# Optimization experiments

Hardware: AMD Instinct MI355X
Metric: run time of the kernel (lower is better)

The kernel has to match this reference:

```python
import jax, jax.numpy as jnp
import numpy as np

B, T, IN, H, S, OUT = 128, 512, 64, 1024, 64, 1


def _lstm_cell(x, h, c, Wih, Whh, bih, bhh):
    # PyTorch gate order: i, f, g, o
    z = x @ Wih.T + h @ Whh.T + bih + bhh  # (B, 4H)
    i, f, g, o = jnp.split(z, 4, axis=-1)
    c = jax.nn.sigmoid(f) * c + jax.nn.sigmoid(i) * jnp.tanh(g)
    h = jax.nn.sigmoid(o) * jnp.tanh(c)
    return h, c


def _run_layer(xs, Wih, Whh, bih, bhh):
    # xs: (T, B, in); returns (ys (T,B,H), h_final, c_final)
    b = xs.shape[1]
    h0 = jnp.zeros((b, H), xs.dtype)
    c0 = jnp.zeros((b, H), xs.dtype)

    def step(carry, x):
        h, c = carry
        h, c = _lstm_cell(x, h, c, Wih, Whh, bih, bhh)
        return (h, c), h

    (hf, cf), ys = jax.lax.scan(step, (h0, c0), xs)
    return ys, hf, cf


def setup_inputs() -> dict:
    key = jax.random.key(0)
    ks = jax.random.split(key, 20)
    s = 0.02
    d = {"x": jax.random.normal(ks[0], (B, T, IN), jnp.float32)}
    # encoder params
    d["enc_Wih0"] = jax.random.normal(ks[1], (4 * H, IN), jnp.float32) * s
    d["enc_Whh0"] = jax.random.normal(ks[2], (4 * H, H), jnp.float32) * s
    d["enc_bih0"] = jnp.zeros((4 * H,), jnp.float32)
    d["enc_bhh0"] = jnp.zeros((4 * H,), jnp.float32)
    d["enc_Wih1"] = jax.random.normal(ks[3], (4 * H, H), jnp.float32) * s
    d["enc_Whh1"] = jax.random.normal(ks[4], (4 * H, H), jnp.float32) * s
    d["enc_bih1"] = jnp.zeros((4 * H,), jnp.float32)
    d["enc_bhh1"] = jnp.zeros((4 * H,), jnp.float32)
    # decoder params (input size = OUT = 1)
    d["dec_Wih0"] = jax.random.normal(ks[5], (4 * H, OUT), jnp.float32) * s
    d["dec_Whh0"] = jax.random.normal(ks[6], (4 * H, H), jnp.float32) * s
    d["dec_bih0"] = jnp.zeros((4 * H,), jnp.float32)
    d["dec_bhh0"] = jnp.zeros((4 * H,), jnp.float32)
    d["dec_Wih1"] = jax.random.normal(ks[7], (4 * H, H), jnp.float32) * s
    d["dec_Whh1"] = jax.random.normal(ks[8], (4 * H, H), jnp.float32) * s
    d["dec_bih1"] = jnp.zeros((4 * H,), jnp.float32)
    d["dec_bhh1"] = jnp.zeros((4 * H,), jnp.float32)
    d["fc_W"] = jax.random.normal(ks[9], (OUT, H), jnp.float32) * s
    d["fc_b"] = jnp.zeros((OUT,), jnp.float32)
    return d


def reference(x, enc_Wih0, enc_Whh0, enc_bih0, enc_bhh0,
              enc_Wih1, enc_Whh1, enc_bih1, enc_bhh1,
              dec_Wih0, dec_Whh0, dec_bih0, dec_bhh0,
              dec_Wih1, dec_Whh1, dec_bih1, dec_bhh1,
              fc_W, fc_b):
    b = x.shape[0]
    xs = jnp.transpose(x, (1, 0, 2))  # (T, B, IN)
    # encoder: layer-by-layer
    ys0, h0e, c0e = _run_layer(xs, enc_Wih0, enc_Whh0, enc_bih0, enc_bhh0)
    _, h1e, c1e = _run_layer(ys0, enc_Wih1, enc_Whh1, enc_bih1, enc_bhh1)

    inp0 = jnp.zeros((b, OUT), x.dtype)

    def dec_step(carry, _):
        h0, c0, h1, c1, inp = carry
        h0, c0 = _lstm_cell(inp, h0, c0, dec_Wih0, dec_Whh0, dec_bih0, dec_bhh0)
        h1, c1 = _lstm_cell(h0, h1, c1, dec_Wih1, dec_Whh1, dec_bih1, dec_bhh1)
        out = h1 @ fc_W.T + fc_b  # (B, OUT)
        return (h0, c0, h1, c1, out), out

    _, outs = jax.lax.scan(dec_step, (h0e, c0e, h1e, c1e, inp0), None, length=S)
    return jnp.transpose(outs, (1, 0, 2))  # (B, S, OUT)
```

## Files before the change

### kernel.cpp

```cpp
#include <hip/hip_runtime.h>
#include <cmath>
#include <cstdint>
#include <cstddef>

#define BB   128
#define TT   512
#define INF  64
#define HH   1024
#define NG   4096
#define SS   64
#define NBLK 192
#define NTHR 512

#define SWHI_B 0
#define SLO_B  131072
#define LDS_BYTES 155648

#define LO_SCALE   2048.0f
#define LO_UNSCALE 4.8828125e-4f

typedef __attribute__((ext_vector_type(8))) short sh8;
typedef __attribute__((ext_vector_type(4))) float f32x4;

__device__ __forceinline__ float h2f(unsigned short u) {
  return (float)__builtin_bit_cast(_Float16, u);
}
__device__ __forceinline__ unsigned short f2h(float f) {
  return __builtin_bit_cast(unsigned short, (_Float16)f);
}
__device__ __forceinline__ float sigm(float x) { return 1.f / (1.f + __expf(-x)); }
__device__ __forceinline__ float tanh_f(float x) {
  x = fminf(15.f, fmaxf(-15.f, x));
  const float e = __expf(2.f * x);
  return (e - 1.f) / (e + 1.f);
}
__device__ __forceinline__ sh8 ld8(const unsigned short* p) { return *(const sh8*)p; }

__device__ __forceinline__ void ld8sc(sh8& d, const unsigned short* p) {
  asm volatile("global_load_dwordx4 %0, %1, off sc0 sc1" : "=v"(d) : "v"(p));
}
__device__ __forceinline__ void ldx4sc(f32x4& d, const float* p) {
  asm volatile("global_load_dwordx4 %0, %1, off sc0 sc1" : "=v"(d) : "v"(p));
}
__device__ __forceinline__ void stx4sc(float* p, f32x4 v) {
  asm volatile("global_store_dwordx4 %0, %1, off sc0 sc1" :: "v"(p), "v"(v) : "memory");
}
__device__ __forceinline__ void st16sc(unsigned short* p, unsigned int v) {
  asm volatile("global_store_short %0, %1, off sc0 sc1" :: "v"(p), "v"(v) : "memory");
}
__device__ __forceinline__ void waitvm(int n) {
  if (n == 6)       asm volatile("s_waitcnt vmcnt(6)" ::: "memory");
  else if (n == 3)  asm volatile("s_waitcnt vmcnt(3)" ::: "memory");
  else              asm volatile("s_waitcnt vmcnt(0)" ::: "memory");
  __builtin_amdgcn_sched_barrier(0);
}

__device__ __forceinline__ void block_sync_lds() {
  asm volatile("s_waitcnt lgkmcnt(0)" ::: "memory");
  __builtin_amdgcn_s_barrier();
  asm volatile("" ::: "memory");
}

#if defined(__HIP_DEVICE_COMPILE__)
typedef __attribute__((ext_vector_type(8))) _Float16 hf8;
template <class T> T&& my_declval();
template <class V, class = void> struct mfma_takes { static constexpr bool value = false; };
template <class V>
struct mfma_takes<V, decltype((void)__builtin_amdgcn_mfma_f32_16x16x32_f16(
                        my_declval<V>(), my_declval<V>(), my_declval<f32x4>(), 0, 0, 0))> {
  static constexpr bool value = true;
};
template <class V>
__device__ __forceinline__ f32x4 mfma_imp(V a, V b, f32x4 c) {
  return __builtin_amdgcn_mfma_f32_16x16x32_f16(a, b, c, 0, 0, 0);
}
__device__ __forceinline__ f32x4 mfma_f16(sh8 a, sh8 b, f32x4 c) {
  if constexpr (mfma_takes<sh8>::value) {
    return mfma_imp<sh8>(a, b, c);
  } else {
    return mfma_imp<hf8>(__builtin_bit_cast(hf8, a), __builtin_bit_cast(hf8, b), c);
  }
}
#else
__device__ __forceinline__ f32x4 mfma_f16(sh8, sh8, f32x4 c) { return c; }
#endif

__global__ __launch_bounds__(256) void prep_weight(const float* __restrict__ W,
                                                   unsigned short* __restrict__ hi,
                                                   unsigned short* __restrict__ lo,
                                                   int lk) {
  const int K = 1 << lk;
  const int idx = blockIdx.x * 256 + threadIdx.x;
  if (idx >= (NG << lk)) return;
  const int n = idx >> lk;
  const int k = idx & (K - 1);
  const float v = W[idx];
  const unsigned short h = f2h(v);
  const unsigned short l = f2h((v - h2f(h)) * LO_SCALE);
  const int nkch = K >> 5;
  const size_t o =
      ((((size_t)(n >> 4) * nkch + (k >> 5)) * 64) + (((k >> 3) & 3) * 16) + (n & 15)) * 8 +
      (k & 7);
  hi[o] = h;
  lo[o] = l;
}

__global__ __launch_bounds__(256) void prep_bias(const float* __restrict__ a,
                                                 const float* __restrict__ b,
                                                 float* __restrict__ o) {
  const int i = blockIdx.x * 256 + threadIdx.x;
  if (i < NG) o[i] = a[i] + b[i];
}

__global__ __launch_bounds__(256) void init_out(float* __restrict__ out_tmp,
                                                const float* __restrict__ fcb) {
  const int i = blockIdx.x * 256 + threadIdx.x;
  if (i < SS * BB) out_tmp[i] = fcb[0];
}

struct KArgs {
  const float* x;
  const unsigned short *wih0_h, *wih0_l;
  const unsigned short *whh0e_h, *whh0e_l;
  const unsigned short *wih1e_h, *wih1e_l;
  const unsigned short *whh1e_h, *whh1e_l;
  const unsigned short *whh0d_h, *whh0d_l;
  const unsigned short *wih1d_h, *wih1d_l;
  const unsigned short *whh1d_h, *whh1d_l;
  const float *bias0e, *bias1e, *bias0d, *bias1d;
  const float *w0col, *fcw, *fcb;
  unsigned short *h00, *h01;
  unsigned short *h10, *h11;
  float *zb0, *zb1;
  float *out_tmp;
  float *outp;
  int *arrive;
};

__device__ __forceinline__ void gbar(int* arrive, int it) {
  asm volatile("s_waitcnt vmcnt(0)" ::: "memory");
  __syncthreads();
  const int tid = threadIdx.x;
  if (tid == 0)
    __hip_atomic_store(&arrive[blockIdx.x * 16], it, __ATOMIC_RELAXED, __HIP_MEMORY_SCOPE_AGENT);
  if (tid < NBLK) {
    while (__hip_atomic_load(&arrive[tid * 16], __ATOMIC_RELAXED, __HIP_MEMORY_SCOPE_AGENT) < it)
      __builtin_amdgcn_s_sleep(1);
  }
  __syncthreads();
  asm volatile("" ::: "memory");
}

__device__ __forceinline__ void load_whi(unsigned short* lds, const unsigned short* hi, int jt) {
#pragma unroll
  for (int g = 0; g < 4; ++g) {
    const uint4* src = (const uint4*)(hi + ((size_t)(g * 64 + jt) * 32) * 512);
    uint4* dst = (uint4*)((char*)lds + SWHI_B + g * 32768);
    for (int u = threadIdx.x; u < 2048; u += NTHR) dst[u] = src[u];
  }
}

__device__ __forceinline__ const unsigned short* lo_src(const unsigned short* glo, int jt,
                                                        int c, int f) {
  const int g = f >> 7, rem = f & 127, kcl = rem >> 6, l = rem & 63;
  const size_t u16 = ((size_t)((g * 64 + jt) * 32) + c * 2 + kcl) * 64 + l;
  return glo + u16 * 8;
}

__device__ __forceinline__ void issue_chunk(const unsigned short* arh,
                                            const unsigned short* glo, int jt, int c, int kg,
                                            int tid, int wid, unsigned short* lds,
                                            sh8 (&AH)[2]) {
#pragma unroll
  for (int kcl = 0; kcl < 2; ++kcl)
    ld8sc(AH[kcl], arh + c * 64 + kcl * 32 + kg * 8);
  __builtin_amdgcn_global_load_lds(
      (const void*)lo_src(glo, jt, c, tid),
      (void*)((char*)lds + SLO_B + (c % 3) * 8192 + wid * 1024), 16, 0, 0);
}

__device__ __forceinline__ void compute_chunk(f32x4* acc, f32x4* accL,
                                              const unsigned short* lds, int c, int lane,
                                              const sh8 (&AH)[2]) {
#pragma unroll
  for (int kcl = 0; kcl < 2; ++kcl) {
    const int kc = c * 2 + kcl;
#pragma unroll
    for (int g = 0; g < 4; ++g) {
      const sh8 bH = ld8(lds + (g * 32 + kc) * 512 + lane * 8);
      const sh8 bL = ld8(lds + SLO_B / 2 + (c % 3) * 4096 + (g * 2 + kcl) * 512 + lane * 8);
      acc[g] = mfma_f16(AH[kcl], bH, acc[g]);
      accL[g] = mfma_f16(AH[kcl], bL, accL[g]);
    }
  }
}

__device__ __forceinline__ void gemm1024(f32x4* acc, f32x4* accL,
                                         const unsigned short* __restrict__ ah,
                                         const unsigned short* __restrict__ glo,
                                         int jt, unsigned short* lds) {
  const int tid = threadIdx.x;
  const int lane = tid & 63, wid = tid >> 6;
  const int kg = lane >> 4;
  const int arow = wid * 16 + (lane & 15);
  const unsigned short* arh = ah + (size_t)arow * HH;

  sh8 AH[3][2];

  asm volatile("s_waitcnt vmcnt(0)" ::: "memory");
  issue_chunk(arh, glo, jt, 0, kg, tid, wid, lds, AH[0]);
  issue_chunk(arh, glo, jt, 1, kg, tid, wid, lds, AH[1]);
  issue_chunk(arh, glo, jt, 2, kg, tid, wid, lds, AH[2]);
  waitvm(6);
  block_sync_lds();

#pragma unroll
  for (int c = 0; c < 16; ++c) {
    compute_chunk(acc, accL, lds, c, lane, AH[c % 3]);
    if (c < 15) {
      waitvm(c <= 13 ? 3 : 0);
      block_sync_lds();
      if (c + 3 < 16)
        issue_chunk(arh, glo, jt, c + 3, kg, tid, wid, lds, AH[c % 3]);
    }
  }
}

__device__ __forceinline__ void combine(f32x4* acc, const f32x4* accL) {
#pragma unroll
  for (int g = 0; g < 4; ++g) acc[g] += accL[g] * LO_UNSCALE;
}

__device__ __forceinline__ void gemm_x(f32x4* acc, f32x4* accL, const float* __restrict__ x,
                                       int t, const unsigned short* __restrict__ wxh,
                                       const unsigned short* __restrict__ wxl, int jt) {
  const int tid = threadIdx.x;
  const int lane = tid & 63, wid = tid >> 6;
  const int kg = lane >> 4;
  const int arow = wid * 16 + (lane & 15);
  const float* xr = x + (size_t)arow * (TT * INF) + t * INF;
#pragma unroll
  for (int kc2 = 0; kc2 < 2; ++kc2) {
    const int kb = kc2 * 32 + kg * 8;
    sh8 xh, xl;
#pragma unroll
    for (int e = 0; e < 8; ++e) {
      const float v = xr[kb + e];
      const unsigned short h = f2h(v);
      xh[e] = (short)h;
      xl[e] = (short)f2h((v - h2f(h)) * LO_SCALE);
    }
#pragma unroll
    for (int g = 0; g < 4; ++g) {
      const size_t bo = (((size_t)(g * 64 + jt) * 2 + kc2) * 64 + lane) * 8;
      const sh8 bH = ld8(wxh + bo);
      const sh8 bL = ld8(wxl + bo);
      acc[g] = mfma_f16(xh, bH, acc[g]);
      accL[g] = mfma_f16(xl, bH, accL[g]);
      accL[g] = mfma_f16(xh, bL, accL[g]);
    }
  }
}

__device__ __forceinline__ void store_z(f32x4* acc, float* zb, int jt) {
  const int tid = threadIdx.x;
  const int lane = tid & 63, wid = tid >> 6;
  const int col = lane & 15, kg = lane >> 4;
#pragma unroll
  for (int g = 0; g < 4; ++g) {
    const int row = g * HH + jt * 16 + col;
    const int bq = wid * 16 + kg * 4;
    stx4sc(zb + (size_t)row * BB + bq, acc[g]);
  }
}
__device__ __forceinline__ void add_z(f32x4* acc, const float* zb, int jt) {
  const int tid = threadIdx.x;
  const int lane = tid & 63, wid = tid >> 6;
  const int col = lane & 15, kg = lane >> 4;
  f32x4 t0, t1, t2, t3;
  const int bq = wid * 16 + kg * 4;
  ldx4sc(t0, zb + (size_t)(0 * HH + jt * 16 + col) * BB + bq);
  ldx4sc(t1, zb + (size_t)(1 * HH + jt * 16 + col) * BB + bq);
  ldx4sc(t2, zb + (size_t)(2 * HH + jt * 16 + col) * BB + bq);
  ldx4sc(t3, zb + (size_t)(3 * HH + jt * 16 + col) * BB + bq);
  asm volatile("s_waitcnt vmcnt(0)" ::: "memory");
  __builtin_amdgcn_sched_barrier(0);
  acc[0] += t0;
  acc[1] += t1;
  acc[2] += t2;
  acc[3] += t3;
}

template <int MODE>
__device__ __forceinline__ void cellfin(f32x4* acc, float* creg,
                                        const float* __restrict__ bias, int jt,
                                        unsigned short* __restrict__ nh,
                                        const float* w0g, const float* inp_vec, float fcwj,
                                        float* fc_out) {
  const int tid = threadIdx.x;
  const int lane = tid & 63, wid = tid >> 6;
  const int col = lane & 15, kg = lane >> 4;
  const int j = jt * 16 + col;
  const float b0 = bias[j], b1 = bias[HH + j], b2 = bias[2 * HH + j], b3 = bias[3 * HH + j];
#pragma unroll
  for (int r = 0; r < 4; ++r) {
    const int b = wid * 16 + kg * 4 + r;
    float zi = acc[0][r] + b0;
    float zf = acc[1][r] + b1;
    float zg = acc[2][r] + b2;
    float zo = acc[3][r] + b3;
    if constexpr (MODE == 1) {
      const float ip = inp_vec
          ? __hip_atomic_load(inp_vec + b, __ATOMIC_RELAXED, __HIP_MEMORY_SCOPE_AGENT)
          : 0.f;
      zi += ip * w0g[0];
      zf += ip * w0g[1];
      zg += ip * w0g[2];
      zo += ip * w0g[3];
    }
    const float cn = sigm(zf) * creg[r] + sigm(zi) * tanh_f(zg);
    const float hn = sigm(zo) * tanh_f(cn);
    creg[r] = cn;
    st16sc(nh + (size_t)b * HH + j, f2h(hn));
    if constexpr (MODE == 2) {
      float cb = hn * fcwj;
      cb += __shfl_xor(cb, 1);
      cb += __shfl_xor(cb, 2);
      cb += __shfl_xor(cb, 4);
      cb += __shfl_xor(cb, 8);
      if (col == 0) atomicAdd(fc_out + b, cb);
    }
  }
}

__device__ __forceinline__ void zacc(f32x4* acc) {
#pragma unroll
  for (int g = 0; g < 4; ++g) acc[g] = f32x4{0.f, 0.f, 0.f, 0.f};
}

__global__ __launch_bounds__(NTHR, 2) void seq2seq_coop(KArgs a) {
  extern __shared__ unsigned short lds[];
  const int bid = blockIdx.x;
  const int role = bid >> 6;
  const int jt = bid & 63;
  const int tid = threadIdx.x;
  int bseq = 0;

  unsigned short* h0[2] = {a.h00, a.h01};
  unsigned short* h1[2] = {a.h10, a.h11};
  float* zb[2] = {a.zb0, a.zb1};

  if (role == 0) load_whi(lds, a.whh0e_h, jt);
  else if (role == 1) load_whi(lds, a.wih1e_h, jt);
  else load_whi(lds, a.whh1e_h, jt);
  __syncthreads();

  float creg[4] = {};

  for (int i = 0; i < TT + 2; ++i) {
    if (role == 0) {
      if (i < TT) {
        f32x4 acc[4], accL[4];
        zacc(acc);
        zacc(accL);
        gemm1024(acc, accL, h0[(i + 1) & 1], a.whh0e_l, jt, lds);
        gemm_x(acc, accL, a.x, i, a.wih0_h, a.wih0_l, jt);
        combine(acc, accL);
        cellfin<0>(acc, creg, a.bias0e, jt, h0[i & 1], nullptr, nullptr, 0.f, nullptr);
      }
    } else if (role == 1) {
      if (i >= 1 && i <= TT) {
        const int s = i - 1;
        f32x4 acc[4], accL[4];
        zacc(acc);
        zacc(accL);
        gemm1024(acc, accL, h0[s & 1], a.wih1e_l, jt, lds);
        combine(acc, accL);
        store_z(acc, zb[s & 1], jt);
      }
    } else {
      if (i >= 2) {
        const int s = i - 2;
        f32x4 acc[4], accL[4];
        zacc(acc);
        zacc(accL);
        gemm1024(acc, accL, h1[(s + 1) & 1], a.whh1e_l, jt, lds);
        combine(acc, accL);
        add_z(acc, zb[s & 1], jt);
        cellfin<0>(acc, creg, a.bias1e, jt, h1[s & 1], nullptr, nullptr, 0.f, nullptr);
      }
    }
    gbar(a.arrive, ++bseq);
  }

  if (role == 0) load_whi(lds, a.whh0d_h, jt);
  else if (role == 1) load_whi(lds, a.wih1d_h, jt);
  else load_whi(lds, a.whh1d_h, jt);
  __syncthreads();

  float w0g[4] = {0.f, 0.f, 0.f, 0.f};
  float fcwj = 0.f;
  if (role == 0) {
    const int j = jt * 16 + (tid & 15);
    w0g[0] = a.w0col[j];
    w0g[1] = a.w0col[HH + j];
    w0g[2] = a.w0col[2 * HH + j];
    w0g[3] = a.w0col[3 * HH + j];
  }
  if (role == 2) fcwj = a.fcw[jt * 16 + (tid & 15)];

  for (int s = 0; s < SS; ++s) {
    f32x4 acc2[4], accL2[4];
    if (role == 2) {
      zacc(acc2);
      zacc(accL2);
      gemm1024(acc2, accL2, h1[(s + 1) & 1], a.whh1d_l, jt, lds);
      combine(acc2, accL2);
    }
    if (role == 0) {
      f32x4 acc[4], accL[4];
      zacc(acc);
      zacc(accL);
      gemm1024(acc, accL, h0[(s + 1) & 1], a.whh0d_l, jt, lds);
      combine(acc, accL);
      cellfin<1>(acc, creg, a.bias0d, jt, h0[s & 1], w0g,
                 s ? a.out_tmp + (s - 1) * BB : nullptr, 0.f, nullptr);
    }
    gbar(a.arrive, ++bseq);
    if (role == 1) {
      f32x4 acc[4], accL[4];
      zacc(acc);
      zacc(accL);
      gemm1024(acc, accL, h0[s & 1], a.wih1d_l, jt, lds);
      combine(acc, accL);
      store_z(acc, zb[0], jt);
    }
    gbar(a.arrive, ++bseq);
    if (role == 2) {
      add_z(acc2, zb[0], jt);
      cellfin<2>(acc2, creg, a.bias1d, jt, h1[s & 1], nullptr, nullptr, fcwj,
                 a.out_tmp + s * BB);
    }
    gbar(a.arrive, ++bseq);
  }

  if (bid < 16) {
    const int gi = bid * NTHR + tid;
    const int b = gi >> 6, s2 = gi & 63;
    a.outp[gi] =
        __hip_atomic_load(a.out_tmp + s2 * BB + b, __ATOMIC_RELAXED, __HIP_MEMORY_SCOPE_AGENT);
  }
}

extern "C" void kernel_launch(void* const* d_in, const int* in_sizes, int n_in,
                              void* d_out, int out_size, void* d_ws, size_t ws_size,
                              hipStream_t stream) {
  (void)in_sizes; (void)n_in; (void)out_size; (void)ws_size;
  const float* x     = (const float*)d_in[0];
  const float* eWih0 = (const float*)d_in[1];
  const float* eWhh0 = (const float*)d_in[2];
  const float* eBih0 = (const float*)d_in[3];
  const float* eBhh0 = (const float*)d_in[4];
  const float* eWih1 = (const float*)d_in[5];
  const float* eWhh1 = (const float*)d_in[6];
  const float* eBih1 = (const float*)d_in[7];
  const float* eBhh1 = (const float*)d_in[8];
  const float* dWih0 = (const float*)d_in[9];
  const float* dWhh0 = (const float*)d_in[10];
  const float* dBih0 = (const float*)d_in[11];
  const float* dBhh0 = (const float*)d_in[12];
  const float* dWih1 = (const float*)d_in[13];
  const float* dWhh1 = (const float*)d_in[14];
  const float* dBih1 = (const float*)d_in[15];
  const float* dBhh1 = (const float*)d_in[16];
  const float* fcW   = (const float*)d_in[17];
  const float* fcB   = (const float*)d_in[18];
  float* out = (float*)d_out;

  char* base = (char*)d_ws;
  size_t off = 0;
  auto alloc = [&](size_t bytes) -> void* {
    void* p = base + off;
    off = (off + bytes + 255) & ~(size_t)255;
    return p;
  };

  unsigned short* h00 = (unsigned short*)alloc(BB * HH * 2);
  unsigned short* h01 = (unsigned short*)alloc(BB * HH * 2);
  unsigned short* h10 = (unsigned short*)alloc(BB * HH * 2);
  unsigned short* h11 = (unsigned short*)alloc(BB * HH * 2);
  int* bar = (int*)alloc(NBLK * 16 * sizeof(int));
  const size_t zbytes = off;

  float* zb0 = (float*)alloc((size_t)NG * BB * 4);
  float* zb1 = (float*)alloc((size_t)NG * BB * 4);
  float* out_tmp = (float*)alloc(SS * BB * 4);

  unsigned short* wih0_h = (unsigned short*)alloc((size_t)NG * INF * 2);
  unsigned short* wih0_l = (unsigned short*)alloc((size_t)NG * INF * 2);
  auto big = [&]() { return (unsigned short*)alloc((size_t)NG * HH * 2); };
  unsigned short *whh0e_h = big(), *whh0e_l = big();
  unsigned short *wih1e_h = big(), *wih1e_l = big();
  unsigned short *whh1e_h = big(), *whh1e_l = big();
  unsigned short *whh0d_h = big(), *whh0d_l = big();
  unsigned short *wih1d_h = big(), *wih1d_l = big();
  unsigned short *whh1d_h = big(), *whh1d_l = big();
  float* bias0e = (float*)alloc(NG * 4);
  float* bias1e = (float*)alloc(NG * 4);
  float* bias0d = (float*)alloc(NG * 4);
  float* bias1d = (float*)alloc(NG * 4);

  (void)hipMemsetAsync(base, 0, zbytes, stream);
  const int gb = (NG * HH + 255) / 256;
  prep_weight<<<gb, 256, 0, stream>>>(eWhh0, whh0e_h, whh0e_l, 10);
  prep_weight<<<gb, 256, 0, stream>>>(eWih1, wih1e_h, wih1e_l, 10);
  prep_weight<<<gb, 256, 0, stream>>>(eWhh1, whh1e_h, whh1e_l, 10);
  prep_weight<<<gb, 256, 0, stream>>>(dWhh0, whh0d_h, whh0d_l, 10);
  prep_weight<<<gb, 256, 0, stream>>>(dWih1, wih1d_h, wih1d_l, 10);
  prep_weight<<<gb, 256, 0, stream>>>(dWhh1, whh1d_h, whh1d_l, 10);
  prep_weight<<<(NG * INF + 255) / 256, 256, 0, stream>>>(eWih0, wih0_h, wih0_l, 6);
  const int gbias = (NG + 255) / 256;
  prep_bias<<<gbias, 256, 0, stream>>>(eBih0, eBhh0, bias0e);
  prep_bias<<<gbias, 256, 0, stream>>>(eBih1, eBhh1, bias1e);
  prep_bias<<<gbias, 256, 0, stream>>>(dBih0, dBhh0, bias0d);
  prep_bias<<<gbias, 256, 0, stream>>>(dBih1, dBhh1, bias1d);
  init_out<<<(SS * BB + 255) / 256, 256, 0, stream>>>(out_tmp, fcB);

  KArgs ka;
  ka.x = x;
  ka.wih0_h = wih0_h; ka.wih0_l = wih0_l;
  ka.whh0e_h = whh0e_h; ka.whh0e_l = whh0e_l;
  ka.wih1e_h = wih1e_h; ka.wih1e_l = wih1e_l;
  ka.whh1e_h = whh1e_h; ka.whh1e_l = whh1e_l;
  ka.whh0d_h = whh0d_h; ka.whh0d_l = whh0d_l;
  ka.wih1d_h = wih1d_h; ka.wih1d_l = wih1d_l;
  ka.whh1d_h = whh1d_h; ka.whh1d_l = whh1d_l;
  ka.bias0e = bias0e; ka.bias1e = bias1e; ka.bias0d = bias0d; ka.bias1d = bias1d;
  ka.w0col = dWih0; ka.fcw = fcW; ka.fcb = fcB;
  ka.h00 = h00; ka.h01 = h01; ka.h10 = h10; ka.h11 = h11;
  ka.zb0 = zb0; ka.zb1 = zb1;
  ka.out_tmp = out_tmp;
  ka.outp = out;
  ka.arrive = bar;

  (void)hipFuncSetAttribute((const void*)seq2seq_coop,
                            hipFuncAttributeMaxDynamicSharedMemorySize, LDS_BYTES);
  seq2seq_coop<<<dim3(NBLK), dim3(NTHR), LDS_BYTES, stream>>>(ka);
}
```

Before: 10.41 ms.

## Drop fp16 low-part weight correction and simplify GEMM pipeline to register-only prefetch

Removes the split-precision (hi+lo fp16) weight representation for the recurrent matrices, so each step runs one MFMA per tile instead of two. The per-chunk streaming of low-part weights into LDS and the block-wide barriers that guarded it are removed. The A-operand prefetch becomes four chunks deep, and compute is wrapped in s_setprio. Weight accuracy drops to plain fp16 (the input x keeps a hi/lo split), so numerical error accumulated over 512+64 recurrent steps may grow against the fp32 reference.

Measured after the change: 8.411 ms (median of 2 runs). 19.2% less time.

```diff
diff --git a/kernel.cpp b/kernel.cpp
--- a/kernel.cpp
+++ b/kernel.cpp
@@ -12,12 +12,7 @@
 #define NBLK 192
 #define NTHR 512
 
-#define SWHI_B 0
-#define SLO_B  131072
-#define LDS_BYTES 155648
-
-#define LO_SCALE   2048.0f
-#define LO_UNSCALE 4.8828125e-4f
+#define LDS_BYTES 131072
 
 typedef __attribute__((ext_vector_type(8))) short sh8;
 typedef __attribute__((ext_vector_type(4))) float f32x4;
@@ -50,15 +45,10 @@
 }
 __device__ __forceinline__ void waitvm(int n) {
   if (n == 6)       asm volatile("s_waitcnt vmcnt(6)" ::: "memory");
-  else if (n == 3)  asm volatile("s_waitcnt vmcnt(3)" ::: "memory");
+  else if (n == 4)  asm volatile("s_waitcnt vmcnt(4)" ::: "memory");
+  else if (n == 2)  asm volatile("s_waitcnt vmcnt(2)" ::: "memory");
   else              asm volatile("s_waitcnt vmcnt(0)" ::: "memory");
   __builtin_amdgcn_sched_barrier(0);
-}
-
-__device__ __forceinline__ void block_sync_lds() {
-  asm volatile("s_waitcnt lgkmcnt(0)" ::: "memory");
-  __builtin_amdgcn_s_barrier();
-  asm volatile("" ::: "memory");
 }
 
 #if defined(__HIP_DEVICE_COMPILE__)
@@ -87,22 +77,17 @@
 
 __global__ __launch_bounds__(256) void prep_weight(const float* __restrict__ W,
                                                    unsigned short* __restrict__ hi,
-                                                   unsigned short* __restrict__ lo,
                                                    int lk) {
   const int K = 1 << lk;
   const int idx = blockIdx.x * 256 + threadIdx.x;
   if (idx >= (NG << lk)) return;
   const int n = idx >> lk;
   const int k = idx & (K - 1);
-  const float v = W[idx];
-  const unsigned short h = f2h(v);
-  const unsigned short l = f2h((v - h2f(h)) * LO_SCALE);
   const int nkch = K >> 5;
   const size_t o =
       ((((size_t)(n >> 4) * nkch + (k >> 5)) * 64) + (((k >> 3) & 3) * 16) + (n & 15)) * 8 +
       (k & 7);
-  hi[o] = h;
-  lo[o] = l;
+  hi[o] = f2h(W[idx]);
 }
 
 __global__ __launch_bounds__(256) void prep_bias(const float* __restrict__ a,
@@ -120,13 +105,13 @@
 
 struct KArgs {
   const float* x;
-  const unsigned short *wih0_h, *wih0_l;
-  const unsigned short *whh0e_h, *whh0e_l;
-  const unsigned short *wih1e_h, *wih1e_l;
-  const unsigned short *whh1e_h, *whh1e_l;
-  const unsigned short *whh0d_h, *whh0d_l;
-  const unsigned short *wih1d_h, *wih1d_l;
-  const unsigned short *whh1d_h, *whh1d_l;
+  const unsigned short* wih0_h;
+  const unsigned short* whh0e_h;
+  const unsigned short* wih1e_h;
+  const unsigned short* whh1e_h;
+  const unsigned short* whh0d_h;
+  const unsigned short* wih1d_h;
+  const unsigned short* whh1d_h;
   const float *bias0e, *bias1e, *bias0d, *bias1d;
   const float *w0col, *fcw, *fcb;
   unsigned short *h00, *h01;
@@ -155,85 +140,61 @@
 #pragma unroll
   for (int g = 0; g < 4; ++g) {
     const uint4* src = (const uint4*)(hi + ((size_t)(g * 64 + jt) * 32) * 512);
-    uint4* dst = (uint4*)((char*)lds + SWHI_B + g * 32768);
+    uint4* dst = (uint4*)(lds + g * 16384);
     for (int u = threadIdx.x; u < 2048; u += NTHR) dst[u] = src[u];
   }
 }
 
-__device__ __forceinline__ const unsigned short* lo_src(const unsigned short* glo, int jt,
-                                                        int c, int f) {
-  const int g = f >> 7, rem = f & 127, kcl = rem >> 6, l = rem & 63;
-  const size_t u16 = ((size_t)((g * 64 + jt) * 32) + c * 2 + kcl) * 64 + l;
-  return glo + u16 * 8;
-}
-
-__device__ __forceinline__ void issue_chunk(const unsigned short* arh,
-                                            const unsigned short* glo, int jt, int c, int kg,
-                                            int tid, int wid, unsigned short* lds,
+__device__ __forceinline__ void issue_chunk(const unsigned short* arh, int c, int kg,
                                             sh8 (&AH)[2]) {
 #pragma unroll
   for (int kcl = 0; kcl < 2; ++kcl)
     ld8sc(AH[kcl], arh + c * 64 + kcl * 32 + kg * 8);
-  __builtin_amdgcn_global_load_lds(
-      (const void*)lo_src(glo, jt, c, tid),
-      (void*)((char*)lds + SLO_B + (c % 3) * 8192 + wid * 1024), 16, 0, 0);
-}
-
-__device__ __forceinline__ void compute_chunk(f32x4* acc, f32x4* accL,
-                                              const unsigned short* lds, int c, int lane,
-                                              const sh8 (&AH)[2]) {
+}
+
+__device__ __forceinline__ void compute_chunk(f32x4* acc, const unsigned short* lds, int c,
+                                              int lane, const sh8 (&AH)[2]) {
+  __builtin_amdgcn_s_setprio(1);
 #pragma unroll
   for (int kcl = 0; kcl < 2; ++kcl) {
     const int kc = c * 2 + kcl;
 #pragma unroll
     for (int g = 0; g < 4; ++g) {
       const sh8 bH = ld8(lds + (g * 32 + kc) * 512 + lane * 8);
-      const sh8 bL = ld8(lds + SLO_B / 2 + (c % 3) * 4096 + (g * 2 + kcl) * 512 + lane * 8);
       acc[g] = mfma_f16(AH[kcl], bH, acc[g]);
-      accL[g] = mfma_f16(AH[kcl], bL, accL[g]);
-    }
-  }
-}
-
-__device__ __forceinline__ void gemm1024(f32x4* acc, f32x4* accL,
+    }
+  }
+  __builtin_amdgcn_s_setprio(0);
+}
+
+__device__ __forceinline__ void gemm1024(f32x4* acc,
                                          const unsigned short* __restrict__ ah,
-                                         const unsigned short* __restrict__ glo,
-                                         int jt, unsigned short* lds) {
+                                         const unsigned short* lds) {
   const int tid = threadIdx.x;
   const int lane = tid & 63, wid = tid >> 6;
   const int kg = lane >> 4;
   const int arow = wid * 16 + (lane & 15);
   const unsigned short* arh = ah + (size_t)arow * HH;
 
-  sh8 AH[3][2];
+  sh8 AH[4][2];
 
   asm volatile("s_waitcnt vmcnt(0)" ::: "memory");
-  issue_chunk(arh, glo, jt, 0, kg, tid, wid, lds, AH[0]);
-  issue_chunk(arh, glo, jt, 1, kg, tid, wid, lds, AH[1]);
-  issue_chunk(arh, glo, jt, 2, kg, tid, wid, lds, AH[2]);
-  waitvm(6);
-  block_sync_lds();
+  issue_chunk(arh, 0, kg, AH[0]);
+  issue_chunk(arh, 1, kg, AH[1]);
+  issue_chunk(arh, 2, kg, AH[2]);
+  issue_chunk(arh, 3, kg, AH[3]);
 
 #pragma unroll
   for (int c = 0; c < 16; ++c) {
-    compute_chunk(acc, accL, lds, c, lane, AH[c % 3]);
-    if (c < 15) {
-      waitvm(c <= 13 ? 3 : 0);
-      block_sync_lds();
-      if (c + 3 < 16)
-        issue_chunk(arh, glo, jt, c + 3, kg, tid, wid, lds, AH[c % 3]);
-    }
-  }
-}
-
-__device__ __forceinline__ void combine(f32x4* acc, const f32x4* accL) {
-#pragma unroll
-  for (int g = 0; g < 4; ++g) acc[g] += accL[g] * LO_UNSCALE;
-}
-
-__device__ __forceinline__ void gemm_x(f32x4* acc, f32x4* accL, const float* __restrict__ x,
-                                       int t, const unsigned short* __restrict__ wxh,
-                                       const unsigned short* __restrict__ wxl, int jt) {
+    const int rem = (c + 3 < 16) ? 3 : (15 - c);
+    waitvm(rem * 2);
+    compute_chunk(acc, lds, c, lane, AH[c % 4]);
+    if (c + 4 < 16) issue_chunk(arh, c + 4, kg, AH[c % 4]);
+  }
+}
+
+__device__ __forceinline__ void gemm_x(f32x4* acc, const float* __restrict__ x, int t,
+                                       const unsigned short* __restrict__ wxh, int jt) {
   const int tid = threadIdx.x;
   const int lane = tid & 63, wid = tid >> 6;
   const int kg = lane >> 4;
@@ -248,16 +209,14 @@
       const float v = xr[kb + e];
       const unsigned short h = f2h(v);
       xh[e] = (short)h;
-      xl[e] = (short)f2h((v - h2f(h)) * LO_SCALE);
+      xl[e] = (short)f2h(v - h2f(h));
     }
 #pragma unroll
     for (int g = 0; g < 4; ++g) {
       const size_t bo = (((size_t)(g * 64 + jt) * 2 + kc2) * 64 + lane) * 8;
       const sh8 bH = ld8(wxh + bo);
-      const sh8 bL = ld8(wxl + bo);
       acc[g] = mfma_f16(xh, bH, acc[g]);
-      accL[g] = mfma_f16(xl, bH, accL[g]);
-      accL[g] = mfma_f16(xh, bL, accL[g]);
+      acc[g] = mfma_f16(xl, bH, acc[g]);
     }
   }
 }
@@ -360,32 +319,26 @@
   for (int i = 0; i < TT + 2; ++i) {
     if (role == 0) {
       if (i < TT) {
-        f32x4 acc[4], accL[4];
+        f32x4 acc[4];
         zacc(acc);
-        zacc(accL);
-        gemm1024(acc, accL, h0[(i + 1) & 1], a.whh0e_l, jt, lds);
-        gemm_x(acc, accL, a.x, i, a.wih0_h, a.wih0_l, jt);
-        combine(acc, accL);
+        gemm1024(acc, h0[(i + 1) & 1], lds);
+        gemm_x(acc, a.x, i, a.wih0_h, jt);
         cellfin<0>(acc, creg, a.bias0e, jt, h0[i & 1], nullptr, nullptr, 0.f, nullptr);
       }
     } else if (role == 1) {
       if (i >= 1 && i <= TT) {
         const int s = i - 1;
-        f32x4 acc[4], accL[4];
+        f32x4 acc[4];
         zacc(acc);
-        zacc(accL);
-        gemm1024(acc, accL, h0[s & 1], a.wih1e_l, jt, lds);
-        combine(acc, accL);
+        gemm1024(acc, h0[s & 1], lds);
         store_z(acc, zb[s & 1], jt);
       }
     } else {
       if (i >= 2) {
         const int s = i - 2;
-        f32x4 acc[4], accL[4];
+        f32x4 acc[4];
         zacc(acc);
-        zacc(accL);
-        gemm1024(acc, accL, h1[(s + 1) & 1], a.whh1e_l, jt, lds);
-        combine(acc, accL);
+        gemm1024(acc, h1[(s + 1) & 1], lds);
         add_z(acc, zb[s & 1], jt);
         cellfin<0>(acc, creg, a.bias1e, jt, h1[s & 1], nullptr, nullptr, 0.f, nullptr);
       }
@@ -410,29 +363,23 @@
   if (role == 2) fcwj = a.fcw[jt * 16 + (tid & 15)];
 
   for (int s = 0; s < SS; ++s) {
-    f32x4 acc2[4], accL2[4];
+    f32x4 acc2[4];
     if (role == 2) {
       zacc(acc2);
-      zacc(accL2);
-      gemm1024(acc2, accL2, h1[(s + 1) & 1], a.whh1d_l, jt, lds);
-      combine(acc2, accL2);
+      gemm1024(acc2, h1[(s + 1) & 1], lds);
     }
     if (role == 0) {
-      f32x4 acc[4], accL[4];
+      f32x4 acc[4];
       zacc(acc);
-      zacc(accL);
-      gemm1024(acc, accL, h0[(s + 1) & 1], a.whh0d_l, jt, lds);
-      combine(acc, accL);
+      gemm1024(acc, h0[(s + 1) & 1], lds);
       cellfin<1>(acc, creg, a.bias0d, jt, h0[s & 1], w0g,
                  s ? a.out_tmp + (s - 1) * BB : nullptr, 0.f, nullptr);
     }
     gbar(a.arrive, ++bseq);
     if (role == 1) {
-      f32x4 acc[4], accL[4];
+      f32x4 acc[4];
       zacc(acc);
-      zacc(accL);
-      gemm1024(acc, accL, h0[s & 1], a.wih1d_l, jt, lds);
-      combine(acc, accL);
+      gemm1024(acc, h0[s & 1], lds);
       store_z(acc, zb[0], jt);
     }
     gbar(a.arrive, ++bseq);
@@ -497,14 +444,13 @@
   float* out_tmp = (float*)alloc(SS * BB * 4);
 
   unsigned short* wih0_h = (unsigned short*)alloc((size_t)NG * INF * 2);
-  unsigned short* wih0_l = (unsigned short*)alloc((size_t)NG * INF * 2);
   auto big = [&]() { return (unsigned short*)alloc((size_t)NG * HH * 2); };
-  unsigned short *whh0e_h = big(), *whh0e_l = big();
-  unsigned short *wih1e_h = big(), *wih1e_l = big();
-  unsigned short *whh1e_h = big(), *whh1e_l = big();
-  unsigned short *whh0d_h = big(), *whh0d_l = big();
-  unsigned short *wih1d_h = big(), *wih1d_l = big();
-  unsigned short *whh1d_h = big(), *whh1d_l = big();
+  unsigned short* whh0e_h = big();
+  unsigned short* wih1e_h = big();
+  unsigned short* whh1e_h = big();
+  unsigned short* whh0d_h = big();
+  unsigned short* wih1d_h = big();
+  unsigned short* whh1d_h = big();
   float* bias0e = (float*)alloc(NG * 4);
   float* bias1e = (float*)alloc(NG * 4);
   float* bias0d = (float*)alloc(NG * 4);
@@ -512,13 +458,13 @@
 
   (void)hipMemsetAsync(base, 0, zbytes, stream);
   const int gb = (NG * HH + 255) / 256;
-  prep_weight<<<gb, 256, 0, stream>>>(eWhh0, whh0e_h, whh0e_l, 10);
-  prep_weight<<<gb, 256, 0, stream>>>(eWih1, wih1e_h, wih1e_l, 10);
-  prep_weight<<<gb, 256, 0, stream>>>(eWhh1, whh1e_h, whh1e_l, 10);
-  prep_weight<<<gb, 256, 0, stream>>>(dWhh0, whh0d_h, whh0d_l, 10);
-  prep_weight<<<gb, 256, 0, stream>>>(dWih1, wih1d_h, wih1d_l, 10);
-  prep_weight<<<gb, 256, 0, stream>>>(dWhh1, whh1d_h, whh1d_l, 10);
-  prep_weight<<<(NG * INF + 255) / 256, 256, 0, stream>>>(eWih0, wih0_h, wih0_l, 6);
+  prep_weight<<<gb, 256, 0, stream>>>(eWhh0, whh0e_h, 10);
+  prep_weight<<<gb, 256, 0, stream>>>(eWih1, wih1e_h, 10);
+  prep_weight<<<gb, 256, 0, stream>>>(eWhh1, whh1e_h, 10);
+  prep_weight<<<gb, 256, 0, stream>>>(dWhh0, whh0d_h, 10);
+  prep_weight<<<gb, 256, 0, stream>>>(dWih1, wih1d_h, 10);
+  prep_weight<<<gb, 256, 0, stream>>>(dWhh1, whh1d_h, 10);
+  prep_weight<<<(NG * INF + 255) / 256, 256, 0, stream>>>(eWih0, wih0_h, 6);
   const int gbias = (NG + 255) / 256;
   prep_bias<<<gbias, 256, 0, stream>>>(eBih0, eBhh0, bias0e);
   prep_bias<<<gbias, 256, 0, stream>>>(eBih1, eBhh1, bias1e);
@@ -528,13 +474,13 @@
 
   KArgs ka;
   ka.x = x;
-  ka.wih0_h = wih0_h; ka.wih0_l = wih0_l;
-  ka.whh0e_h = whh0e_h; ka.whh0e_l = whh0e_l;
-  ka.wih1e_h = wih1e_h; ka.wih1e_l = wih1e_l;
-  ka.whh1e_h = whh1e_h; ka.whh1e_l = whh1e_l;
-  ka.whh0d_h = whh0d_h; ka.whh0d_l = whh0d_l;
-  ka.wih1d_h = wih1d_h; ka.wih1d_l = wih1d_l;
-  ka.whh1d_h = whh1d_h; ka.whh1d_l = whh1d_l;
+  ka.wih0_h = wih0_h;
+  ka.whh0e_h = whh0e_h;
+  ka.wih1e_h = wih1e_h;
+  ka.whh1e_h = whh1e_h;
+  ka.whh0d_h = whh0d_h;
+  ka.wih1d_h = wih1d_h;
+  ka.whh1d_h = whh1d_h;
   ka.bias0e = bias0e; ka.bias1e = bias1e; ka.bias0d = bias0d; ka.bias1d = bias1d;
   ka.w0col = dWih0; ka.fcw = fcW; ka.fcb = fcB;
   ka.h00 = h00; ka.h01 = h01; ka.h10 = h10; ka.h11 = h11;
```
